# Performance work log

Measured on AMD Instinct MI355X. Metric: run time of the kernel, lower is better.

## Reference

```python
import jax, jax.numpy as jnp
import numpy as np
from jax import lax

E = 3  # num_experts

def _maxpool2(x):
    return lax.reduce_window(x, -jnp.inf, lax.max, (1, 1, 2, 2), (1, 1, 2, 2), 'VALID')

def _mixed_conv(x, experts, routing, stride, pad):
    # per-sample expert-mixed convolution via grouped conv trick
    B, Ci, H, W = x.shape
    _, Co, _, k, _ = experts.shape
    kern = jnp.einsum('be,eoikl->boikl', routing, experts).reshape(B * Co, Ci, k, k)
    y = lax.conv_general_dilated(
        x.reshape(1, B * Ci, H, W), kern, (stride, stride),
        [(pad, pad), (pad, pad)],
        dimension_numbers=('NCHW', 'OIHW', 'NCHW'),
        feature_group_count=B)
    return y.reshape(B, Co, y.shape[2], y.shape[3])

def _dyres_conv(x, experts, rw, rb, stride=1, pad=1):
    # DyRes mode 'A': routing from avg-pool + spatial-std descriptors, softmax over experts
    avg = x.mean((2, 3))
    std = x.std((2, 3))
    r = jax.nn.softmax((avg + std) @ rw.T + rb, axis=-1)  # [B, E]
    return _mixed_conv(x, experts, r, stride, pad)

def _cond_conv(x, experts, rw, rb, stride=1, pad=1):
    # CondConv: sigmoid routing from global average pool
    r = jax.nn.sigmoid(x.mean((2, 3)) @ rw.T + rb)  # [B, E]
    return _mixed_conv(x, experts, r, stride, pad)

def _conv_init(key, co, ci, k):
    return jax.random.normal(key, (E, co, ci, k, k), jnp.float32) * np.sqrt(2.0 / (ci * k * k)).astype(np.float32)

def setup_inputs() -> dict:
    key = jax.random.key(0)
    ks = jax.random.split(key, 20)
    B = 512
    d = {}
    d['x'] = jax.random.normal(ks[0], (B, 3, 32, 32), jnp.float32)
    d['dw1'] = _conv_init(ks[1], 64, 3, 3)
    d['rw1'] = jax.random.normal(ks[2], (E, 3), jnp.float32) * 0.1
    d['rb1'] = jnp.zeros((E,), jnp.float32)
    d['dw2'] = _conv_init(ks[3], 192, 64, 3)
    d['rw2'] = jax.random.normal(ks[4], (E, 64), jnp.float32) * 0.1
    d['rb2'] = jnp.zeros((E,), jnp.float32)
    d['dw3'] = _conv_init(ks[5], 384, 192, 3)
    d['rw3'] = jax.random.normal(ks[6], (E, 192), jnp.float32) * 0.1
    d['rb3'] = jnp.zeros((E,), jnp.float32)
    d['cw4'] = _conv_init(ks[7], 256, 384, 3)
    d['cr4w'] = jax.random.normal(ks[8], (E, 384), jnp.float32) * 0.1
    d['cr4b'] = jnp.zeros((E,), jnp.float32)
    d['cw5'] = _conv_init(ks[9], 256, 256, 3)
    d['cr5w'] = jax.random.normal(ks[10], (E, 256), jnp.float32) * 0.1
    d['cr5b'] = jnp.zeros((E,), jnp.float32)
    d['fw1'] = jax.random.normal(ks[11], (4096, 1024), jnp.float32) * np.sqrt(2.0 / 1024).astype(np.float32)
    d['fb1'] = jnp.zeros((4096,), jnp.float32)
    d['fw2'] = jax.random.normal(ks[12], (4096, 4096), jnp.float32) * np.sqrt(2.0 / 4096).astype(np.float32)
    d['fb2'] = jnp.zeros((4096,), jnp.float32)
    d['fw3'] = jax.random.normal(ks[13], (100, 4096), jnp.float32) * np.sqrt(1.0 / 4096).astype(np.float32)
    d['fb3'] = jnp.zeros((100,), jnp.float32)
    return d

def reference(x, dw1, rw1, rb1, dw2, rw2, rb2, dw3, rw3, rb3,
              cw4, cr4w, cr4b, cw5, cr5w, cr5b,
              fw1, fb1, fw2, fb2, fw3, fb3):
    h = jax.nn.relu(_dyres_conv(x, dw1, rw1, rb1, stride=2))   # [B,64,16,16]
    h = _maxpool2(h)                                           # [B,64,8,8]
    h = jax.nn.relu(_dyres_conv(h, dw2, rw2, rb2))             # [B,192,8,8]
    h = _maxpool2(h)                                           # [B,192,4,4]
    h = jax.nn.relu(_dyres_conv(h, dw3, rw3, rb3))             # [B,384,4,4]
    h = jax.nn.relu(_cond_conv(h, cw4, cr4w, cr4b))            # [B,256,4,4]
    h = jax.nn.relu(_cond_conv(h, cw5, cr5w, cr5b))            # [B,256,4,4]
    h = _maxpool2(h)                                           # [B,256,2,2]
    h = h.reshape(h.shape[0], -1)                              # [B,1024]
    h = jax.nn.relu(h @ fw1.T + fb1)
    h = jax.nn.relu(h @ fw2.T + fb2)
    return h @ fw3.T + fb3                                     # [B,100]
```

## Files before the change

### kernel.cpp

```cpp
#include <hip/hip_runtime.h>
#include <math.h>


typedef unsigned short u16;
typedef unsigned int u32;
typedef short bf16x8 __attribute__((ext_vector_type(8)));
typedef float f32x4 __attribute__((ext_vector_type(4)));

__device__ __forceinline__ u16 bf16_rne(float f) {
    u32 u = __float_as_uint(f);
    return (u16)((u + 0x7fffu + ((u >> 16) & 1u)) >> 16);
}
__device__ __forceinline__ u32 packsplit(float v) {
    u16 h = bf16_rne(v);
    float hf = __uint_as_float((u32)h << 16);
    u16 l = bf16_rne(v - hf);
    return ((u32)h << 16) | l;
}
__device__ __forceinline__ float unpackf(u32 p) {
    return __uint_as_float(p & 0xffff0000u) + __uint_as_float(p << 16);
}

__global__ __launch_bounds__(256)
void wsplit_kernel(const float* __restrict__ W, u16* __restrict__ whi,
                   u16* __restrict__ wlo, int total, int Kper, int Kpad)
{
    int idx = blockIdx.x * 256 + threadIdx.x;
    if (idx >= total) return;
    int r = idx / Kpad, k = idx - r * Kpad;
    float v = (k < Kper) ? W[(size_t)r * Kper + k] : 0.f;
    u16 h = bf16_rne(v);
    whi[idx] = h;
    wlo[idx] = bf16_rne(v - __uint_as_float((u32)h << 16));
}

__global__ __launch_bounds__(64)
void stats_kernel(const void* __restrict__ actv, float* __restrict__ s,
                  int Bsz, int C, int HW, int cbhw, int use_std, int packed)
{
    int idx = blockIdx.x;
    int b = idx / C, c = idx - b * C;
    size_t base = (cbhw ? ((size_t)c * Bsz + b) : ((size_t)b * C + c)) * HW;
    int lane = threadIdx.x;
    float sum = 0.f, sq = 0.f;
    if (packed) {
        const u32* p = (const u32*)actv + base;
        for (int i = lane; i < HW; i += 64) { float v = unpackf(p[i]); sum += v; sq += v * v; }
    } else {
        const float* p = (const float*)actv + base;
        for (int i = lane; i < HW; i += 64) { float v = p[i]; sum += v; sq += v * v; }
    }
#pragma unroll
    for (int off = 32; off > 0; off >>= 1) {
        sum += __shfl_down(sum, off);
        sq  += __shfl_down(sq, off);
    }
    if (lane == 0) {
        float inv = 1.f / (float)HW;
        float mean = sum * inv;
        float var = sq * inv - mean * mean;
        float outv = mean;
        if (use_std) outv += sqrtf(fmaxf(var, 0.f));
        s[idx] = outv;
    }
}

__global__ __launch_bounds__(64)
void routing_kernel(const float* __restrict__ s, const float* __restrict__ rw,
                    const float* __restrict__ rb, float* __restrict__ r,
                    int C, int softmax_mode)
{
    int b = blockIdx.x;
    int lane = threadIdx.x;
    float d0 = 0.f, d1 = 0.f, d2 = 0.f;
    for (int c = lane; c < C; c += 64) {
        float sv = s[b * C + c];
        d0 += sv * rw[c];
        d1 += sv * rw[C + c];
        d2 += sv * rw[2 * C + c];
    }
#pragma unroll
    for (int off = 32; off > 0; off >>= 1) {
        d0 += __shfl_down(d0, off);
        d1 += __shfl_down(d1, off);
        d2 += __shfl_down(d2, off);
    }
    if (lane == 0) {
        d0 += rb[0]; d1 += rb[1]; d2 += rb[2];
        if (softmax_mode) {
            float mx = fmaxf(d0, fmaxf(d1, d2));
            float e0 = expf(d0 - mx), e1 = expf(d1 - mx), e2 = expf(d2 - mx);
            float inv = 1.f / (e0 + e1 + e2);
            r[b * 3 + 0] = e0 * inv;
            r[b * 3 + 1] = e1 * inv;
            r[b * 3 + 2] = e2 * inv;
        } else {
            r[b * 3 + 0] = 1.f / (1.f + expf(-d0));
            r[b * 3 + 1] = 1.f / (1.f + expf(-d1));
            r[b * 3 + 2] = 1.f / (1.f + expf(-d2));
        }
    }
}

template<int BMODE>
__global__ __launch_bounds__(256, 2)
void cgemm_kernel(const u16* __restrict__ Whi, const u16* __restrict__ Wlo,
                  const u32* __restrict__ Bpk, const float* __restrict__ rptr,
                  float* __restrict__ Cout,
                  int M, int N, int Kper, int Kpad, int Kchunk,
                  int Ci, int Bsz, int H, int W, int lgS, int lgOW, int stride)
{
    __shared__ __align__(16) u16 Ah[2][128 * 40], Al[2][128 * 40];
    __shared__ __align__(16) u16 Bh[2][128 * 40], Bl[2][128 * 40];
    const int tid = threadIdx.x;
    const int n0 = blockIdx.x << 7, m0 = blockIdx.y << 7;
    const int kq0 = blockIdx.z * Kchunk;

    const int rowA = tid >> 1, kh16 = (tid & 1) << 4;
    const int nB = tid & 127, kOff = (tid >> 7) << 4;

    const int nn = n0 + nB;
    const int bB = nn >> lgS;
    const int sidx = nn & ((1 << lgS) - 1);
    const int ohs = (sidx >> lgOW) * stride - 1;
    const int ows = (sidx & ((1 << lgOW) - 1)) * stride - 1;
    const int chanStride = (BMODE == 2) ? H * W : Bsz * H * W;
    const long bOff = (BMODE == 2) ? (long)bB * Ci * H * W : (long)bB * H * W;
    const long nBase = bOff + (long)ohs * W + ows;

    const int lane = tid & 63, wv = tid >> 6;
    const int lm = lane & 15, qd = lane >> 4;
    const int wm = (wv & 1) << 6, wn = (wv >> 1) << 6;

    float rsv[3][4];
#pragma unroll
    for (int ni = 0; ni < 4; ++ni) {
        int n = n0 + wn + ni * 16 + lm;
        int b = n >> lgS;
#pragma unroll
        for (int e = 0; e < 3; ++e) rsv[e][ni] = rptr[b * 3 + e];
    }

    f32x4 acc[4][4], accS[4][4];
#pragma unroll
    for (int i = 0; i < 4; ++i)
#pragma unroll
        for (int j = 0; j < 4; ++j) {
            acc[i][j]  = (f32x4){0.f, 0.f, 0.f, 0.f};
            accS[i][j] = (f32x4){0.f, 0.f, 0.f, 0.f};
        }

    const int mg = m0 + rowA;
    const int nkz = Kchunk >> 5;
    const int NS = 3 * nkz;

    int eL = 0, kL = kq0;
    uint4 pA0, pA1, pA2, pA3;
    u32 pB[16];

    auto LOAD = [&]() {
        size_t aOff = ((size_t)(eL * M + mg)) * Kpad + kL + kh16;
        const u16* hp = Whi + aOff;
        const u16* lp = Wlo + aOff;
        pA0 = *(const uint4*)hp; pA1 = *(const uint4*)(hp + 8);
        pA2 = *(const uint4*)lp; pA3 = *(const uint4*)(lp + 8);
        int kb = kL + kOff;
#pragma unroll
        for (int j = 0; j < 16; ++j) {
            int k = kb + j;
            int ci = (int)((unsigned)k / 9u);
            int r9 = k - ci * 9;
            int kh = (int)(((unsigned)r9 * 11u) >> 5);
            int kw = r9 - kh * 3;
            int ih = ohs + kh, iw = ows + kw;
            u32 p = 0;
            if (k < Kper && (unsigned)ih < (unsigned)H && (unsigned)iw < (unsigned)W)
                p = Bpk[nBase + (long)ci * chanStride + kh * W + kw];
            pB[j] = p;
        }
    };
    auto ADV = [&]() {
        kL += 32;
        if (kL == kq0 + Kchunk) { kL = kq0; ++eL; }
    };
    auto STORE = [&](int buf) {
        *(uint4*)(&Ah[buf][rowA * 40 + kh16])     = pA0;
        *(uint4*)(&Ah[buf][rowA * 40 + kh16 + 8]) = pA1;
        *(uint4*)(&Al[buf][rowA * 40 + kh16])     = pA2;
        *(uint4*)(&Al[buf][rowA * 40 + kh16 + 8]) = pA3;
        u32 hw[8], lw[8];
#pragma unroll
        for (int j = 0; j < 8; ++j) {
            u32 p0 = pB[2 * j], p1 = pB[2 * j + 1];
            hw[j] = (p0 >> 16) | (p1 & 0xffff0000u);
            lw[j] = (p0 & 0xffffu) | (p1 << 16);
        }
        *(uint4*)(&Bh[buf][nB * 40 + kOff])     = make_uint4(hw[0], hw[1], hw[2], hw[3]);
        *(uint4*)(&Bh[buf][nB * 40 + kOff + 8]) = make_uint4(hw[4], hw[5], hw[6], hw[7]);
        *(uint4*)(&Bl[buf][nB * 40 + kOff])     = make_uint4(lw[0], lw[1], lw[2], lw[3]);
        *(uint4*)(&Bl[buf][nB * 40 + kOff + 8]) = make_uint4(lw[4], lw[5], lw[6], lw[7]);
    };
    auto COMPUTE = [&](int buf) {
        bf16x8 ah[4], al[4];
#pragma unroll
        for (int mi = 0; mi < 4; ++mi) {
            int row = wm + mi * 16 + lm;
            ah[mi] = *(const bf16x8*)(&Ah[buf][row * 40 + qd * 8]);
            al[mi] = *(const bf16x8*)(&Al[buf][row * 40 + qd * 8]);
        }
        __builtin_amdgcn_s_setprio(1);
#pragma unroll
        for (int ni = 0; ni < 4; ++ni) {
            int row = wn + ni * 16 + lm;
            bf16x8 bh = *(const bf16x8*)(&Bh[buf][row * 40 + qd * 8]);
            bf16x8 bl = *(const bf16x8*)(&Bl[buf][row * 40 + qd * 8]);
#pragma unroll
            for (int mi = 0; mi < 4; ++mi) {
                f32x4 c = acc[mi][ni];
                c = __builtin_amdgcn_mfma_f32_16x16x32_bf16(al[mi], bh, c, 0, 0, 0);
                c = __builtin_amdgcn_mfma_f32_16x16x32_bf16(ah[mi], bl, c, 0, 0, 0);
                c = __builtin_amdgcn_mfma_f32_16x16x32_bf16(ah[mi], bh, c, 0, 0, 0);
                acc[mi][ni] = c;
            }
        }
        __builtin_amdgcn_s_setprio(0);
    };

    LOAD(); ADV();
    int s = 0, buf = 0;
#pragma unroll
    for (int e = 0; e < 3; ++e) {
        for (int t = 0; t < nkz; ++t) {
            STORE(buf);
            if (s + 1 < NS) { LOAD(); ADV(); }
            asm volatile("s_waitcnt lgkmcnt(0)\n\ts_barrier" ::: "memory");
            COMPUTE(buf);
            buf ^= 1; ++s;
        }
#pragma unroll
        for (int mi = 0; mi < 4; ++mi)
#pragma unroll
            for (int ni = 0; ni < 4; ++ni) {
                accS[mi][ni] += acc[mi][ni] * rsv[e][ni];
                acc[mi][ni] = (f32x4){0.f, 0.f, 0.f, 0.f};
            }
    }

    const bool atom = (gridDim.z > 1);
#pragma unroll
    for (int ni = 0; ni < 4; ++ni) {
        int n = n0 + wn + ni * 16 + lm;
#pragma unroll
        for (int mi = 0; mi < 4; ++mi)
#pragma unroll
            for (int r = 0; r < 4; ++r) {
                int m = m0 + wm + mi * 16 + qd * 4 + r;
                if (m >= M) continue;
                float v = accS[mi][ni][r];
                if (atom) atomicAdd(&Cout[(size_t)m * N + n], v);
                else      Cout[(size_t)m * N + n] = v;
            }
    }
}

template<int BMODE, int BIAS, int TROUT>
__global__ __launch_bounds__(256)
void mgemm_kernel(const u16* __restrict__ Whi, const u16* __restrict__ Wlo,
                  const u32* __restrict__ Bpk, const int2* __restrict__ ktab,
                  const float* __restrict__ rptr, const float* __restrict__ bias,
                  float* __restrict__ Cout,
                  int M, int N, int Kpad, int Kchunk, int zpe,
                  int Ci, int Bsz, int H, int W, int lgS, int lgOW, int stride)
{
    __shared__ __align__(16) u16 Ah[128 * 40], Al[128 * 40];
    __shared__ __align__(16) u32 Bp[128 * 36];
    const int tid = threadIdx.x;
    const int n0 = blockIdx.x << 7, m0 = blockIdx.y << 7;
    const int bz = blockIdx.z;
    const int eA = bz / zpe;
    const int kq0 = (bz - eA * zpe) * Kchunk;

    const int rowA = tid >> 1, kh16 = (tid & 1) << 4;
    const int nB = tid & 127, kOff = (tid >> 7) << 4;

    const int lane = tid & 63, wv = tid >> 6;
    const int lm = lane & 15, qd = lane >> 4;
    const int wm = (wv & 1) << 6, wn = (wv >> 1) << 6;

    f32x4 acc[4][4];
#pragma unroll
    for (int i = 0; i < 4; ++i)
#pragma unroll
        for (int j = 0; j < 4; ++j)
            acc[i][j] = (f32x4){0.f, 0.f, 0.f, 0.f};

    const size_t aRowBase = (size_t)eA * M;

    for (int kq = kq0; kq < kq0 + Kchunk; kq += 32) {
        {
            int mg = m0 + rowA;
            uint4 h0 = {0,0,0,0}, h1 = {0,0,0,0}, l0 = {0,0,0,0}, l1 = {0,0,0,0};
            if (mg < M) {
                const u16* hp = Whi + (aRowBase + mg) * Kpad + kq + kh16;
                const u16* lp = Wlo + (aRowBase + mg) * Kpad + kq + kh16;
                h0 = *(const uint4*)hp; h1 = *(const uint4*)(hp + 8);
                l0 = *(const uint4*)lp; l1 = *(const uint4*)(lp + 8);
            }
            *(uint4*)(&Ah[rowA * 40 + kh16])     = h0;
            *(uint4*)(&Ah[rowA * 40 + kh16 + 8]) = h1;
            *(uint4*)(&Al[rowA * 40 + kh16])     = l0;
            *(uint4*)(&Al[rowA * 40 + kh16 + 8]) = l1;
        }
        {
            const u32* bp = Bpk + (size_t)(n0 + nB) * Kpad + kq + kOff;
            uint4 q0 = *(const uint4*)bp;
            uint4 q1 = *(const uint4*)(bp + 4);
            uint4 q2 = *(const uint4*)(bp + 8);
            uint4 q3 = *(const uint4*)(bp + 12);
            *(uint4*)(&Bp[nB * 36 + kOff])      = q0;
            *(uint4*)(&Bp[nB * 36 + kOff + 4])  = q1;
            *(uint4*)(&Bp[nB * 36 + kOff + 8])  = q2;
            *(uint4*)(&Bp[nB * 36 + kOff + 12]) = q3;
        }
        __syncthreads();
        {
            bf16x8 ah[4], al[4];
#pragma unroll
            for (int mi = 0; mi < 4; ++mi) {
                int row = wm + mi * 16 + lm;
                ah[mi] = *(const bf16x8*)(&Ah[row * 40 + qd * 8]);
                al[mi] = *(const bf16x8*)(&Al[row * 40 + qd * 8]);
            }
#pragma unroll
            for (int ni = 0; ni < 4; ++ni) {
                int row = wn + ni * 16 + lm;
                const u32* bp = &Bp[row * 36 + qd * 8];
                uint4 p0 = *(const uint4*)bp;
                uint4 p1 = *(const uint4*)(bp + 4);
                union { u32 w[4]; bf16x8 v; } bh, bl;
                bh.w[0] = (p0.x >> 16) | (p0.y & 0xffff0000u);
                bl.w[0] = (p0.x & 0xffffu) | (p0.y << 16);
                bh.w[1] = (p0.z >> 16) | (p0.w & 0xffff0000u);
                bl.w[1] = (p0.z & 0xffffu) | (p0.w << 16);
                bh.w[2] = (p1.x >> 16) | (p1.y & 0xffff0000u);
                bl.w[2] = (p1.x & 0xffffu) | (p1.y << 16);
                bh.w[3] = (p1.z >> 16) | (p1.w & 0xffff0000u);
                bl.w[3] = (p1.z & 0xffffu) | (p1.w << 16);
#pragma unroll
                for (int mi = 0; mi < 4; ++mi) {
                    f32x4 c = acc[mi][ni];
                    c = __builtin_amdgcn_mfma_f32_16x16x32_bf16(al[mi], bh.v, c, 0, 0, 0);
                    c = __builtin_amdgcn_mfma_f32_16x16x32_bf16(ah[mi], bl.v, c, 0, 0, 0);
                    c = __builtin_amdgcn_mfma_f32_16x16x32_bf16(ah[mi], bh.v, c, 0, 0, 0);
                    acc[mi][ni] = c;
                }
            }
        }
        __syncthreads();
    }

#pragma unroll
    for (int ni = 0; ni < 4; ++ni) {
        int n = n0 + wn + ni * 16 + lm;
        if (n >= N) continue;
#pragma unroll
        for (int mi = 0; mi < 4; ++mi)
#pragma unroll
            for (int r = 0; r < 4; ++r) {
                int m = m0 + wm + mi * 16 + qd * 4 + r;
                if (m >= M) continue;
                float v = acc[mi][ni][r];
                if (BIAS && bz == 0) v += bias[m];
                if (TROUT) atomicAdd(&Cout[(size_t)n * M + m], v);
                else       atomicAdd(&Cout[(size_t)m * N + n], v);
            }
    }
}

__global__ __launch_bounds__(256)
void pack_kernel(const float* __restrict__ in, u32* __restrict__ outp,
                 int count, int relu)
{
    int i = blockIdx.x * 256 + threadIdx.x;
    if (i >= count) return;
    float v = in[i];
    if (relu) v = fmaxf(v, 0.f);
    outp[i] = packsplit(v);
}

template<int RELU>
__global__ __launch_bounds__(256)
void pool_pack_kernel(const float* __restrict__ in, u32* __restrict__ outp,
                      int CB, int H, int W)
{
    int OH = H >> 1, OW = W >> 1;
    int total = CB * OH * OW;
    int i = blockIdx.x * 256 + threadIdx.x;
    if (i >= total) return;
    int ow = i % OW;
    int t = i / OW;
    int oh = t % OH;
    int cb = t / OH;
    const float* p = in + ((size_t)cb * H + (oh << 1)) * W + (ow << 1);
    float v = fmaxf(fmaxf(p[0], p[1]), fmaxf(p[W], p[W + 1]));
    if (RELU) v = fmaxf(v, 0.f);
    outp[i] = packsplit(v);
}

__global__ __launch_bounds__(256)
void pool_flatten_pack_kernel(const float* __restrict__ in, u32* __restrict__ outp)
{
    int i = blockIdx.x * 256 + threadIdx.x;
    if (i >= 512 * 1024) return;
    int b = i >> 10;
    int f = i & 1023;
    int c = f >> 2, s = f & 3;
    int oh = s >> 1, ow = s & 1;
    const float* p = in + (((size_t)c * 512 + b) * 4 + (oh << 1)) * 4 + (ow << 1);
    float v = fmaxf(fmaxf(p[0], p[1]), fmaxf(p[4], p[5]));
    outp[i] = packsplit(fmaxf(v, 0.f));
}

__global__ __launch_bounds__(256)
void tp_pack_kernel(const float* __restrict__ in, u32* __restrict__ outp,
                    int Mt, int Nt)
{
    __shared__ float t[32][33];
    int tx = threadIdx.x & 31, ty = threadIdx.x >> 5;
    int mB = blockIdx.x << 5, nB = blockIdx.y << 5;
#pragma unroll
    for (int i = 0; i < 4; ++i) {
        int mm = ty + i * 8;
        t[mm][tx] = in[(size_t)(mB + mm) * Nt + nB + tx];
    }
    __syncthreads();
#pragma unroll
    for (int i = 0; i < 4; ++i) {
        int nn = ty + i * 8;
        float v = fmaxf(t[tx][nn], 0.f);
        outp[(size_t)(nB + nn) * Mt + mB + tx] = packsplit(v);
    }
}

extern "C" void kernel_launch(void* const* d_in, const int* in_sizes, int n_in,
                              void* d_out, int out_size, void* d_ws, size_t ws_size,
                              hipStream_t stream)
{
    const float* x    = (const float*)d_in[0];
    const float* dw1  = (const float*)d_in[1];
    const float* rw1  = (const float*)d_in[2];
    const float* rb1  = (const float*)d_in[3];
    const float* dw2  = (const float*)d_in[4];
    const float* rw2  = (const float*)d_in[5];
    const float* rb2  = (const float*)d_in[6];
    const float* dw3  = (const float*)d_in[7];
    const float* rw3  = (const float*)d_in[8];
    const float* rb3  = (const float*)d_in[9];
    const float* cw4  = (const float*)d_in[10];
    const float* cr4w = (const float*)d_in[11];
    const float* cr4b = (const float*)d_in[12];
    const float* cw5  = (const float*)d_in[13];
    const float* cr5w = (const float*)d_in[14];
    const float* cr5b = (const float*)d_in[15];
    const float* fw1  = (const float*)d_in[16];
    const float* fb1  = (const float*)d_in[17];
    const float* fw2  = (const float*)d_in[18];
    const float* fb2  = (const float*)d_in[19];
    const float* fw3  = (const float*)d_in[20];
    const float* fb3  = (const float*)d_in[21];
    float* out = (float*)d_out;

    float* ws    = (float*)d_ws;
    float* r1    = ws;
    float* r2    = r1 + 1536;
    float* r3    = r2 + 1536;
    float* r4    = r3 + 1536;
    float* r5    = r4 + 1536;
    float* sdesc = ws + 8192 + 65536;
    const size_t REGION = 18874368;
    float* region = sdesc + 196608;
    float* slab   = region;
    u16*   regEnd = (u16*)(region + REGION);
    u32*   P1     = (u32*)(region + REGION);
    u32*   P2     = P1 + 3145728;

    u16 *w1h = regEnd - 2*(size_t)6144,     *w1l = regEnd - (size_t)6144;
    u16 *w2h = regEnd - 2*(size_t)331776,   *w2l = regEnd - (size_t)331776;
    u16 *w3h = regEnd - 2*(size_t)1990656,  *w3l = regEnd - (size_t)1990656;
    u16 *w4h = regEnd - 2*(size_t)2654208,  *w4l = regEnd - (size_t)2654208;
    u16 *w5h = regEnd - 2*(size_t)1769472,  *w5l = regEnd - (size_t)1769472;
    u16 *f1h = regEnd - 2*(size_t)4194304,  *f1l = regEnd - (size_t)4194304;
    u16 *f2h = regEnd - 2*(size_t)16777216, *f2l = regEnd - (size_t)16777216;
    u16 *f3h = regEnd - 2*(size_t)409600,   *f3l = regEnd - (size_t)409600;

    u32* xpk   = P1;
    u32* a1pk  = P2;
    u32* a2pk  = P1;
    u32* c3pk  = P2;
    u32* c4pk  = P1;
    u32* hTpk  = P2;
    u32* f1pkT = P1;
    u32* f2pkT = P2;

    const int B = 512;

    pack_kernel<<<6144, 256, 0, stream>>>(x, xpk, 1572864, 0);

    wsplit_kernel<<<24, 256, 0, stream>>>(dw1, w1h, w1l, 6144, 27, 32);
    stats_kernel<<<B * 3, 64, 0, stream>>>(x, sdesc, B, 3, 1024, 0, 1, 0);
    routing_kernel<<<B, 64, 0, stream>>>(sdesc, rw1, rb1, r1, 3, 1);
    cgemm_kernel<2><<<dim3(1024, 1, 1), 256, 0, stream>>>(
        w1h, w1l, xpk, r1, slab, 64, 131072, 27, 32, 32, 3, B, 32, 32, 8, 4, 2);
    pool_pack_kernel<1><<<8192, 256, 0, stream>>>(slab, a1pk, 64 * 512, 16, 16);

    wsplit_kernel<<<1296, 256, 0, stream>>>(dw2, w2h, w2l, 331776, 576, 576);
    stats_kernel<<<B * 64, 64, 0, stream>>>(a1pk, sdesc, B, 64, 64, 1, 1, 1);
    routing_kernel<<<B, 64, 0, stream>>>(sdesc, rw2, rb2, r2, 64, 1);
    cgemm_kernel<1><<<dim3(256, 2, 1), 256, 0, stream>>>(
        w2h, w2l, a1pk, r2, slab, 192, 32768, 576, 576, 576, 64, B, 8, 8, 6, 3, 1);
    pool_pack_kernel<1><<<6144, 256, 0, stream>>>(slab, a2pk, 192 * 512, 8, 8);

    wsplit_kernel<<<7776, 256, 0, stream>>>(dw3, w3h, w3l, 1990656, 1728, 1728);
    stats_kernel<<<B * 192, 64, 0, stream>>>(a2pk, sdesc, B, 192, 16, 1, 1, 1);
    routing_kernel<<<B, 64, 0, stream>>>(sdesc, rw3, rb3, r3, 192, 1);
    hipMemsetAsync(slab, 0, (size_t)384 * 8192 * 4, stream);
    cgemm_kernel<1><<<dim3(64, 3, 2), 256, 0, stream>>>(
        w3h, w3l, a2pk, r3, slab, 384, 8192, 1728, 1728, 864, 192, B, 4, 4, 4, 2, 1);
    pack_kernel<<<12288, 256, 0, stream>>>(slab, c3pk, 3145728, 1);

    wsplit_kernel<<<10368, 256, 0, stream>>>(cw4, w4h, w4l, 2654208, 3456, 3456);
    stats_kernel<<<B * 384, 64, 0, stream>>>(c3pk, sdesc, B, 384, 16, 1, 0, 1);
    routing_kernel<<<B, 64, 0, stream>>>(sdesc, cr4w, cr4b, r4, 384, 0);
    hipMemsetAsync(slab, 0, (size_t)256 * 8192 * 4, stream);
    cgemm_kernel<1><<<dim3(64, 2, 4), 256, 0, stream>>>(
        w4h, w4l, c3pk, r4, slab, 256, 8192, 3456, 3456, 864, 384, B, 4, 4, 4, 2, 1);
    pack_kernel<<<8192, 256, 0, stream>>>(slab, c4pk, 2097152, 1);

    wsplit_kernel<<<6912, 256, 0, stream>>>(cw5, w5h, w5l, 1769472, 2304, 2304);
    stats_kernel<<<B * 256, 64, 0, stream>>>(c4pk, sdesc, B, 256, 16, 1, 0, 1);
    routing_kernel<<<B, 64, 0, stream>>>(sdesc, cr5w, cr5b, r5, 256, 0);
    hipMemsetAsync(slab, 0, (size_t)256 * 8192 * 4, stream);
    cgemm_kernel<1><<<dim3(64, 2, 4), 256, 0, stream>>>(
        w5h, w5l, c4pk, r5, slab, 256, 8192, 2304, 2304, 576, 256, B, 4, 4, 4, 2, 1);

    pool_flatten_pack_kernel<<<2048, 256, 0, stream>>>(slab, hTpk);

    wsplit_kernel<<<16384, 256, 0, stream>>>(fw1, f1h, f1l, 4194304, 1024, 1024);
    hipMemsetAsync(slab, 0, (size_t)4096 * 512 * 4, stream);
    mgemm_kernel<0, 1, 0><<<dim3(4, 32, 8), 256, 0, stream>>>(
        f1h, f1l, hTpk, nullptr, nullptr, fb1, slab, 4096, 512, 1024, 128, 8, 0, 0, 0, 0, 0, 0, 0);
    tp_pack_kernel<<<dim3(128, 16), 256, 0, stream>>>(slab, f1pkT, 4096, 512);

    wsplit_kernel<<<65536, 256, 0, stream>>>(fw2, f2h, f2l, 16777216, 4096, 4096);
    hipMemsetAsync(slab, 0, (size_t)4096 * 512 * 4, stream);
    mgemm_kernel<0, 1, 0><<<dim3(4, 32, 8), 256, 0, stream>>>(
        f2h, f2l, f1pkT, nullptr, nullptr, fb2, slab, 4096, 512, 4096, 512, 8, 0, 0, 0, 0, 0, 0, 0);
    tp_pack_kernel<<<dim3(128, 16), 256, 0, stream>>>(slab, f2pkT, 4096, 512);

    wsplit_kernel<<<1600, 256, 0, stream>>>(fw3, f3h, f3l, 409600, 4096, 4096);
    hipMemsetAsync(out, 0, (size_t)512 * 100 * 4, stream);
    mgemm_kernel<0, 1, 1><<<dim3(4, 1, 32), 256, 0, stream>>>(
        f3h, f3l, f2pkT, nullptr, nullptr, fb3, out, 100, 512, 4096, 128, 32, 0, 0, 0, 0, 0, 0, 0);
}
```

Before: 1.496 ms.

## Switch conv activations to padded channels-last layout with vectorized im2col loads

Conv layers 2-5 now store activations in a zero-padded NHWC packed layout. Weights are reordered so K runs over (cell, channel), which lets each thread fetch 16 contiguous B values with four 16-byte loads instead of 16 bounds-checked scalar gathers with div/mod. The GEMM output is written channels-last, and the pool, pack and stats kernels are rewritten to match. Block indices are also swizzled across XCDs. The trade-off is extra padding memory and a stats kernel that runs one thread per channel with serial loops.

```diff
diff --git a/kernel.cpp b/kernel.cpp
--- a/kernel.cpp
+++ b/kernel.cpp
@@ -19,6 +19,11 @@
 }
 __device__ __forceinline__ float unpackf(u32 p) {
     return __uint_as_float(p & 0xffff0000u) + __uint_as_float(p << 16);
+}
+__device__ __forceinline__ int xcd_swz(int bid, int n) {
+    if ((n & 7) != 0) return bid;
+    int cpx = n >> 3;
+    return (bid & 7) * cpx + (bid >> 3);
 }
 
 __global__ __launch_bounds__(256)
@@ -34,22 +39,31 @@
     wlo[idx] = bf16_rne(v - __uint_as_float((u32)h << 16));
 }
 
+__global__ __launch_bounds__(256)
+void wsplit_cl_kernel(const float* __restrict__ W, u16* __restrict__ whi,
+                      u16* __restrict__ wlo, int total, int Ci)
+{
+    int idx = blockIdx.x * 256 + threadIdx.x;
+    if (idx >= total) return;
+    int Kper = 9 * Ci;
+    int r = idx / Kper, kp = idx - r * Kper;
+    int cell = kp / Ci, ci = kp - cell * Ci;
+    float v = W[(size_t)r * Kper + ci * 9 + cell];
+    u16 h = bf16_rne(v);
+    whi[idx] = h;
+    wlo[idx] = bf16_rne(v - __uint_as_float((u32)h << 16));
+}
+
 __global__ __launch_bounds__(64)
-void stats_kernel(const void* __restrict__ actv, float* __restrict__ s,
-                  int Bsz, int C, int HW, int cbhw, int use_std, int packed)
+void stats_kernel(const float* __restrict__ actv, float* __restrict__ s,
+                  int C, int HW, int use_std)
 {
     int idx = blockIdx.x;
-    int b = idx / C, c = idx - b * C;
-    size_t base = (cbhw ? ((size_t)c * Bsz + b) : ((size_t)b * C + c)) * HW;
+    size_t base = (size_t)idx * HW;
     int lane = threadIdx.x;
     float sum = 0.f, sq = 0.f;
-    if (packed) {
-        const u32* p = (const u32*)actv + base;
-        for (int i = lane; i < HW; i += 64) { float v = unpackf(p[i]); sum += v; sq += v * v; }
-    } else {
-        const float* p = (const float*)actv + base;
-        for (int i = lane; i < HW; i += 64) { float v = p[i]; sum += v; sq += v * v; }
-    }
+    const float* p = actv + base;
+    for (int i = lane; i < HW; i += 64) { float v = p[i]; sum += v; sq += v * v; }
 #pragma unroll
     for (int off = 32; off > 0; off >>= 1) {
         sum += __shfl_down(sum, off);
@@ -63,6 +77,26 @@
         if (use_std) outv += sqrtf(fmaxf(var, 0.f));
         s[idx] = outv;
     }
+}
+
+__global__ __launch_bounds__(384)
+void stats_cl_kernel(const u32* __restrict__ act, float* __restrict__ s,
+                     int H2, int W2, int C, int use_std)
+{
+    int b = blockIdx.x, c = threadIdx.x;
+    int Hin = H2 - 2, Win = W2 - 2;
+    float sum = 0.f, sq = 0.f;
+    for (int h = 0; h < Hin; ++h)
+        for (int w = 0; w < Win; ++w) {
+            float v = unpackf(act[(((size_t)b * H2 + h + 1) * W2 + w + 1) * C + c]);
+            sum += v; sq += v * v;
+        }
+    float inv = 1.f / (float)(Hin * Win);
+    float mean = sum * inv;
+    float var = sq * inv - mean * mean;
+    float outv = mean;
+    if (use_std) outv += sqrtf(fmaxf(var, 0.f));
+    s[b * C + c] = outv;
 }
 
 __global__ __launch_bounds__(64)
@@ -102,31 +136,27 @@
     }
 }
 
-template<int BMODE>
+template<int CI, int H2, int W2, int LGS, int LGOW>
 __global__ __launch_bounds__(256, 2)
-void cgemm_kernel(const u16* __restrict__ Whi, const u16* __restrict__ Wlo,
-                  const u32* __restrict__ Bpk, const float* __restrict__ rptr,
-                  float* __restrict__ Cout,
-                  int M, int N, int Kper, int Kpad, int Kchunk,
-                  int Ci, int Bsz, int H, int W, int lgS, int lgOW, int stride)
+void cgemm_cl_kernel(const u16* __restrict__ Whi, const u16* __restrict__ Wlo,
+                     const u32* __restrict__ Bpk, const float* __restrict__ rptr,
+                     float* __restrict__ Cout, int M, int N, int Kper, int Kchunk)
 {
     __shared__ __align__(16) u16 Ah[2][128 * 40], Al[2][128 * 40];
     __shared__ __align__(16) u16 Bh[2][128 * 40], Bl[2][128 * 40];
     const int tid = threadIdx.x;
-    const int n0 = blockIdx.x << 7, m0 = blockIdx.y << 7;
+    const int bx = xcd_swz(blockIdx.x, gridDim.x);
+    const int n0 = bx << 7, m0 = blockIdx.y << 7;
     const int kq0 = blockIdx.z * Kchunk;
 
     const int rowA = tid >> 1, kh16 = (tid & 1) << 4;
     const int nB = tid & 127, kOff = (tid >> 7) << 4;
 
     const int nn = n0 + nB;
-    const int bB = nn >> lgS;
-    const int sidx = nn & ((1 << lgS) - 1);
-    const int ohs = (sidx >> lgOW) * stride - 1;
-    const int ows = (sidx & ((1 << lgOW) - 1)) * stride - 1;
-    const int chanStride = (BMODE == 2) ? H * W : Bsz * H * W;
-    const long bOff = (BMODE == 2) ? (long)bB * Ci * H * W : (long)bB * H * W;
-    const long nBase = bOff + (long)ohs * W + ows;
+    const int bB = nn >> LGS;
+    const int sidx = nn & ((1 << LGS) - 1);
+    const int oh = sidx >> LGOW, ow = sidx & ((1 << LGOW) - 1);
+    const long nBase = ((long)(bB * H2 + oh) * W2 + ow) * CI;
 
     const int lane = tid & 63, wv = tid >> 6;
     const int lm = lane & 15, qd = lane >> 4;
@@ -136,7 +166,7 @@
 #pragma unroll
     for (int ni = 0; ni < 4; ++ni) {
         int n = n0 + wn + ni * 16 + lm;
-        int b = n >> lgS;
+        int b = n >> LGS;
 #pragma unroll
         for (int e = 0; e < 3; ++e) rsv[e][ni] = rptr[b * 3 + e];
     }
@@ -156,28 +186,24 @@
 
     int eL = 0, kL = kq0;
     uint4 pA0, pA1, pA2, pA3;
-    u32 pB[16];
+    uint4 pQ0, pQ1, pQ2, pQ3;
 
     auto LOAD = [&]() {
-        size_t aOff = ((size_t)(eL * M + mg)) * Kpad + kL + kh16;
+        size_t aOff = ((size_t)(eL * M + mg)) * Kper + kL + kh16;
         const u16* hp = Whi + aOff;
         const u16* lp = Wlo + aOff;
         pA0 = *(const uint4*)hp; pA1 = *(const uint4*)(hp + 8);
         pA2 = *(const uint4*)lp; pA3 = *(const uint4*)(lp + 8);
-        int kb = kL + kOff;
-#pragma unroll
-        for (int j = 0; j < 16; ++j) {
-            int k = kb + j;
-            int ci = (int)((unsigned)k / 9u);
-            int r9 = k - ci * 9;
-            int kh = (int)(((unsigned)r9 * 11u) >> 5);
-            int kw = r9 - kh * 3;
-            int ih = ohs + kh, iw = ows + kw;
-            u32 p = 0;
-            if (k < Kper && (unsigned)ih < (unsigned)H && (unsigned)iw < (unsigned)W)
-                p = Bpk[nBase + (long)ci * chanStride + kh * W + kw];
-            pB[j] = p;
-        }
+        int k = kL + kOff;
+        int cell = k / CI;
+        int ci0 = k - cell * CI;
+        int kh = (cell * 11) >> 5;
+        int kw = cell - kh * 3;
+        const u32* bp = Bpk + (nBase + (long)((kh * W2 + kw) * CI + ci0));
+        pQ0 = *(const uint4*)bp;
+        pQ1 = *(const uint4*)(bp + 4);
+        pQ2 = *(const uint4*)(bp + 8);
+        pQ3 = *(const uint4*)(bp + 12);
     };
     auto ADV = [&]() {
         kL += 32;
@@ -188,10 +214,12 @@
         *(uint4*)(&Ah[buf][rowA * 40 + kh16 + 8]) = pA1;
         *(uint4*)(&Al[buf][rowA * 40 + kh16])     = pA2;
         *(uint4*)(&Al[buf][rowA * 40 + kh16 + 8]) = pA3;
+        u32 qv[16] = {pQ0.x, pQ0.y, pQ0.z, pQ0.w, pQ1.x, pQ1.y, pQ1.z, pQ1.w,
+                      pQ2.x, pQ2.y, pQ2.z, pQ2.w, pQ3.x, pQ3.y, pQ3.z, pQ3.w};
         u32 hw[8], lw[8];
 #pragma unroll
         for (int j = 0; j < 8; ++j) {
-            u32 p0 = pB[2 * j], p1 = pB[2 * j + 1];
+            u32 p0 = qv[2 * j], p1 = qv[2 * j + 1];
             hw[j] = (p0 >> 16) | (p1 & 0xffff0000u);
             lw[j] = (p0 & 0xffffu) | (p1 << 16);
         }
@@ -257,28 +285,170 @@
                 int m = m0 + wm + mi * 16 + qd * 4 + r;
                 if (m >= M) continue;
                 float v = accS[mi][ni][r];
-                if (atom) atomicAdd(&Cout[(size_t)m * N + n], v);
-                else      Cout[(size_t)m * N + n] = v;
-            }
-    }
-}
-
-template<int BMODE, int BIAS, int TROUT>
+                if (atom) atomicAdd(&Cout[(size_t)n * M + m], v);
+                else      Cout[(size_t)n * M + m] = v;
+            }
+    }
+}
+
+__global__ __launch_bounds__(256, 2)
+void cgemm_l1_kernel(const u16* __restrict__ Whi, const u16* __restrict__ Wlo,
+                     const u32* __restrict__ Bpk, const float* __restrict__ rptr,
+                     float* __restrict__ Cout, int M, int N)
+{
+    __shared__ __align__(16) u16 Ah[2][128 * 40], Al[2][128 * 40];
+    __shared__ __align__(16) u16 Bh[2][128 * 40], Bl[2][128 * 40];
+    const int tid = threadIdx.x;
+    const int bx = xcd_swz(blockIdx.x, gridDim.x);
+    const int n0 = bx << 7;
+    const int Kper = 27, Kpad = 32;
+    const int H = 32, W = 32;
+
+    const int rowA = tid >> 1, kh16 = (tid & 1) << 4;
+    const int nB = tid & 127, kOff = (tid >> 7) << 4;
+
+    const int nn = n0 + nB;
+    const int bB = nn >> 8;
+    const int sidx = nn & 255;
+    const int ohs = (sidx >> 4) * 2 - 1;
+    const int ows = (sidx & 15) * 2 - 1;
+    const long nBase = (long)bB * 3072 + (long)ohs * W + ows;
+
+    const int lane = tid & 63, wv = tid >> 6;
+    const int lm = lane & 15, qd = lane >> 4;
+    const int wm = (wv & 1) << 6, wn = (wv >> 1) << 6;
+
+    float rsv[3][4];
+#pragma unroll
+    for (int ni = 0; ni < 4; ++ni) {
+        int n = n0 + wn + ni * 16 + lm;
+        int b = n >> 8;
+#pragma unroll
+        for (int e = 0; e < 3; ++e) rsv[e][ni] = rptr[b * 3 + e];
+    }
+
+    f32x4 acc[4][4], accS[4][4];
+#pragma unroll
+    for (int i = 0; i < 4; ++i)
+#pragma unroll
+        for (int j = 0; j < 4; ++j) {
+            acc[i][j]  = (f32x4){0.f, 0.f, 0.f, 0.f};
+            accS[i][j] = (f32x4){0.f, 0.f, 0.f, 0.f};
+        }
+
+    const int mg = rowA;
+    int eL = 0;
+    uint4 pA0, pA1, pA2, pA3;
+    u32 pB[16];
+
+    auto LOAD = [&]() {
+        size_t aOff = ((size_t)(eL * M + mg)) * Kpad + kh16;
+        const u16* hp = Whi + aOff;
+        const u16* lp = Wlo + aOff;
+        pA0 = *(const uint4*)hp; pA1 = *(const uint4*)(hp + 8);
+        pA2 = *(const uint4*)lp; pA3 = *(const uint4*)(lp + 8);
+#pragma unroll
+        for (int j = 0; j < 16; ++j) {
+            int k = kOff + j;
+            int ci = (int)((unsigned)k / 9u);
+            int r9 = k - ci * 9;
+            int kh = (int)(((unsigned)r9 * 11u) >> 5);
+            int kw = r9 - kh * 3;
+            int ih = ohs + kh, iw = ows + kw;
+            u32 p = 0;
+            if (k < Kper && (unsigned)ih < (unsigned)H && (unsigned)iw < (unsigned)W)
+                p = Bpk[nBase + (long)ci * 1024 + kh * W + kw];
+            pB[j] = p;
+        }
+    };
+    auto STORE = [&](int buf) {
+        *(uint4*)(&Ah[buf][rowA * 40 + kh16])     = pA0;
+        *(uint4*)(&Ah[buf][rowA * 40 + kh16 + 8]) = pA1;
+        *(uint4*)(&Al[buf][rowA * 40 + kh16])     = pA2;
+        *(uint4*)(&Al[buf][rowA * 40 + kh16 + 8]) = pA3;
+        u32 hw[8], lw[8];
+#pragma unroll
+        for (int j = 0; j < 8; ++j) {
+            u32 p0 = pB[2 * j], p1 = pB[2 * j + 1];
+            hw[j] = (p0 >> 16) | (p1 & 0xffff0000u);
+            lw[j] = (p0 & 0xffffu) | (p1 << 16);
+        }
+        *(uint4*)(&Bh[buf][nB * 40 + kOff])     = make_uint4(hw[0], hw[1], hw[2], hw[3]);
+        *(uint4*)(&Bh[buf][nB * 40 + kOff + 8]) = make_uint4(hw[4], hw[5], hw[6], hw[7]);
+        *(uint4*)(&Bl[buf][nB * 40 + kOff])     = make_uint4(lw[0], lw[1], lw[2], lw[3]);
+        *(uint4*)(&Bl[buf][nB * 40 + kOff + 8]) = make_uint4(lw[4], lw[5], lw[6], lw[7]);
+    };
+    auto COMPUTE = [&](int buf) {
+        bf16x8 ah[4], al[4];
+#pragma unroll
+        for (int mi = 0; mi < 4; ++mi) {
+            int row = wm + mi * 16 + lm;
+            ah[mi] = *(const bf16x8*)(&Ah[buf][row * 40 + qd * 8]);
+            al[mi] = *(const bf16x8*)(&Al[buf][row * 40 + qd * 8]);
+        }
+        __builtin_amdgcn_s_setprio(1);
+#pragma unroll
+        for (int ni = 0; ni < 4; ++ni) {
+            int row = wn + ni * 16 + lm;
+            bf16x8 bh = *(const bf16x8*)(&Bh[buf][row * 40 + qd * 8]);
+            bf16x8 bl = *(const bf16x8*)(&Bl[buf][row * 40 + qd * 8]);
+#pragma unroll
+            for (int mi = 0; mi < 4; ++mi) {
+                f32x4 c = acc[mi][ni];
+                c = __builtin_amdgcn_mfma_f32_16x16x32_bf16(al[mi], bh, c, 0, 0, 0);
+                c = __builtin_amdgcn_mfma_f32_16x16x32_bf16(ah[mi], bl, c, 0, 0, 0);
+                c = __builtin_amdgcn_mfma_f32_16x16x32_bf16(ah[mi], bh, c, 0, 0, 0);
+                acc[mi][ni] = c;
+            }
+        }
+        __builtin_amdgcn_s_setprio(0);
+    };
+
+    LOAD(); ++eL;
+    int buf = 0;
+#pragma unroll
+    for (int e = 0; e < 3; ++e) {
+        STORE(buf);
+        if (e < 2) { LOAD(); ++eL; }
+        asm volatile("s_waitcnt lgkmcnt(0)\n\ts_barrier" ::: "memory");
+        COMPUTE(buf);
+        buf ^= 1;
+#pragma unroll
+        for (int mi = 0; mi < 4; ++mi)
+#pragma unroll
+            for (int ni = 0; ni < 4; ++ni) {
+                accS[mi][ni] += acc[mi][ni] * rsv[e][ni];
+                acc[mi][ni] = (f32x4){0.f, 0.f, 0.f, 0.f};
+            }
+    }
+
+#pragma unroll
+    for (int ni = 0; ni < 4; ++ni) {
+        int n = n0 + wn + ni * 16 + lm;
+#pragma unroll
+        for (int mi = 0; mi < 4; ++mi)
+#pragma unroll
+            for (int r = 0; r < 4; ++r) {
+                int m = wm + mi * 16 + qd * 4 + r;
+                if (m >= M) continue;
+                Cout[(size_t)n * M + m] = accS[mi][ni][r];
+            }
+    }
+}
+
+template<int BIAS, int TROUT>
 __global__ __launch_bounds__(256)
 void mgemm_kernel(const u16* __restrict__ Whi, const u16* __restrict__ Wlo,
-                  const u32* __restrict__ Bpk, const int2* __restrict__ ktab,
-                  const float* __restrict__ rptr, const float* __restrict__ bias,
+                  const u32* __restrict__ Bpk, const float* __restrict__ bias,
                   float* __restrict__ Cout,
-                  int M, int N, int Kpad, int Kchunk, int zpe,
-                  int Ci, int Bsz, int H, int W, int lgS, int lgOW, int stride)
+                  int M, int N, int Kpad, int Kchunk)
 {
     __shared__ __align__(16) u16 Ah[128 * 40], Al[128 * 40];
     __shared__ __align__(16) u32 Bp[128 * 36];
     const int tid = threadIdx.x;
     const int n0 = blockIdx.x << 7, m0 = blockIdx.y << 7;
     const int bz = blockIdx.z;
-    const int eA = bz / zpe;
-    const int kq0 = (bz - eA * zpe) * Kchunk;
+    const int kq0 = bz * Kchunk;
 
     const int rowA = tid >> 1, kh16 = (tid & 1) << 4;
     const int nB = tid & 127, kOff = (tid >> 7) << 4;
@@ -293,16 +463,14 @@
 #pragma unroll
         for (int j = 0; j < 4; ++j)
             acc[i][j] = (f32x4){0.f, 0.f, 0.f, 0.f};
-
-    const size_t aRowBase = (size_t)eA * M;
 
     for (int kq = kq0; kq < kq0 + Kchunk; kq += 32) {
         {
             int mg = m0 + rowA;
             uint4 h0 = {0,0,0,0}, h1 = {0,0,0,0}, l0 = {0,0,0,0}, l1 = {0,0,0,0};
             if (mg < M) {
-                const u16* hp = Whi + (aRowBase + mg) * Kpad + kq + kh16;
-                const u16* lp = Wlo + (aRowBase + mg) * Kpad + kq + kh16;
+                const u16* hp = Whi + (size_t)mg * Kpad + kq + kh16;
+                const u16* lp = Wlo + (size_t)mg * Kpad + kq + kh16;
                 h0 = *(const uint4*)hp; h1 = *(const uint4*)(hp + 8);
                 l0 = *(const uint4*)lp; l1 = *(const uint4*)(lp + 8);
             }
@@ -378,46 +546,65 @@
 }
 
 __global__ __launch_bounds__(256)
-void pack_kernel(const float* __restrict__ in, u32* __restrict__ outp,
-                 int count, int relu)
+void pack_kernel(const float* __restrict__ in, u32* __restrict__ outp, int count)
 {
     int i = blockIdx.x * 256 + threadIdx.x;
     if (i >= count) return;
-    float v = in[i];
-    if (relu) v = fmaxf(v, 0.f);
-    outp[i] = packsplit(v);
-}
-
-template<int RELU>
+    outp[i] = packsplit(in[i]);
+}
+
 __global__ __launch_bounds__(256)
-void pool_pack_kernel(const float* __restrict__ in, u32* __restrict__ outp,
-                      int CB, int H, int W)
-{
-    int OH = H >> 1, OW = W >> 1;
-    int total = CB * OH * OW;
+void pool_pack_cl_kernel(const float* __restrict__ in, u32* __restrict__ outp,
+                         int Bn, int Hin, int Win, int C)
+{
+    int OH = Hin >> 1, OW = Win >> 1, H2 = OH + 2, W2 = OW + 2;
+    int total = Bn * H2 * W2 * C;
     int i = blockIdx.x * 256 + threadIdx.x;
     if (i >= total) return;
-    int ow = i % OW;
-    int t = i / OW;
-    int oh = t % OH;
-    int cb = t / OH;
-    const float* p = in + ((size_t)cb * H + (oh << 1)) * W + (ow << 1);
-    float v = fmaxf(fmaxf(p[0], p[1]), fmaxf(p[W], p[W + 1]));
-    if (RELU) v = fmaxf(v, 0.f);
-    outp[i] = packsplit(v);
+    int c = i % C; int t = i / C;
+    int w = t % W2; t /= W2;
+    int h = t % H2; int b = t / H2;
+    u32 pv = 0;
+    if (h >= 1 && h <= OH && w >= 1 && w <= OW) {
+        int oh = h - 1, ow = w - 1;
+        const float* p = in + (((size_t)b * Hin + 2 * oh) * Win + 2 * ow) * C + c;
+        size_t rs = (size_t)Win * C;
+        float v = fmaxf(fmaxf(p[0], p[C]), fmaxf(p[rs], p[rs + C]));
+        pv = packsplit(fmaxf(v, 0.f));
+    }
+    outp[i] = pv;
 }
 
 __global__ __launch_bounds__(256)
-void pool_flatten_pack_kernel(const float* __restrict__ in, u32* __restrict__ outp)
+void pack_cl_kernel(const float* __restrict__ in, u32* __restrict__ outp,
+                    int Bn, int Hin, int Win, int C)
+{
+    int H2 = Hin + 2, W2 = Win + 2;
+    int total = Bn * H2 * W2 * C;
+    int i = blockIdx.x * 256 + threadIdx.x;
+    if (i >= total) return;
+    int c = i % C; int t = i / C;
+    int w = t % W2; t /= W2;
+    int h = t % H2; int b = t / H2;
+    u32 pv = 0;
+    if (h >= 1 && h <= Hin && w >= 1 && w <= Win) {
+        float v = in[(((size_t)b * Hin + (h - 1)) * Win + (w - 1)) * C + c];
+        pv = packsplit(fmaxf(v, 0.f));
+    }
+    outp[i] = pv;
+}
+
+__global__ __launch_bounds__(256)
+void pool_flatten_cl_kernel(const float* __restrict__ in, u32* __restrict__ outp)
 {
     int i = blockIdx.x * 256 + threadIdx.x;
     if (i >= 512 * 1024) return;
     int b = i >> 10;
     int f = i & 1023;
-    int c = f >> 2, s = f & 3;
-    int oh = s >> 1, ow = s & 1;
-    const float* p = in + (((size_t)c * 512 + b) * 4 + (oh << 1)) * 4 + (ow << 1);
-    float v = fmaxf(fmaxf(p[0], p[1]), fmaxf(p[4], p[5]));
+    int c = f >> 2, sp = f & 3;
+    int oh = sp >> 1, ow = sp & 1;
+    const float* p = in + (((size_t)b * 4 + 2 * oh) * 4 + 2 * ow) * 256 + c;
+    float v = fmaxf(fmaxf(p[0], p[256]), fmaxf(p[1024], p[1024 + 256]));
     outp[i] = packsplit(fmaxf(v, 0.f));
 }
 
@@ -480,9 +667,9 @@
     const size_t REGION = 18874368;
     float* region = sdesc + 196608;
     float* slab   = region;
+    u32*   a3u    = (u32*)(region + 4194304);
     u16*   regEnd = (u16*)(region + REGION);
     u32*   P1     = (u32*)(region + REGION);
-    u32*   P2     = P1 + 3145728;
 
     u16 *w1h = regEnd - 2*(size_t)6144,     *w1l = regEnd - (size_t)6144;
     u16 *w2h = regEnd - 2*(size_t)331776,   *w2l = regEnd - (size_t)331776;
@@ -494,71 +681,70 @@
     u16 *f3h = regEnd - 2*(size_t)409600,   *f3l = regEnd - (size_t)409600;
 
     u32* xpk   = P1;
-    u32* a1pk  = P2;
-    u32* a2pk  = P1;
-    u32* c3pk  = P2;
-    u32* c4pk  = P1;
-    u32* hTpk  = P2;
-    u32* f1pkT = P1;
-    u32* f2pkT = P2;
+    u32* a1    = P1;
+    u32* a2    = P1;
+    u32* a4    = P1;
+    u32* hTpk  = P1;
+    u32* f1pkT = P1 + 1048576;
+    u32* f2pkT = P1 + 3145728;
 
     const int B = 512;
 
-    pack_kernel<<<6144, 256, 0, stream>>>(x, xpk, 1572864, 0);
+    pack_kernel<<<6144, 256, 0, stream>>>(x, xpk, 1572864);
 
     wsplit_kernel<<<24, 256, 0, stream>>>(dw1, w1h, w1l, 6144, 27, 32);
-    stats_kernel<<<B * 3, 64, 0, stream>>>(x, sdesc, B, 3, 1024, 0, 1, 0);
+    stats_kernel<<<B * 3, 64, 0, stream>>>(x, sdesc, 3, 1024, 1);
     routing_kernel<<<B, 64, 0, stream>>>(sdesc, rw1, rb1, r1, 3, 1);
-    cgemm_kernel<2><<<dim3(1024, 1, 1), 256, 0, stream>>>(
-        w1h, w1l, xpk, r1, slab, 64, 131072, 27, 32, 32, 3, B, 32, 32, 8, 4, 2);
-    pool_pack_kernel<1><<<8192, 256, 0, stream>>>(slab, a1pk, 64 * 512, 16, 16);
-
-    wsplit_kernel<<<1296, 256, 0, stream>>>(dw2, w2h, w2l, 331776, 576, 576);
-    stats_kernel<<<B * 64, 64, 0, stream>>>(a1pk, sdesc, B, 64, 64, 1, 1, 1);
+    cgemm_l1_kernel<<<dim3(1024, 1, 1), 256, 0, stream>>>(
+        w1h, w1l, xpk, r1, slab, 64, 131072);
+    pool_pack_cl_kernel<<<12800, 256, 0, stream>>>(slab, a1, B, 16, 16, 64);
+
+    wsplit_cl_kernel<<<1296, 256, 0, stream>>>(dw2, w2h, w2l, 331776, 64);
+    stats_cl_kernel<<<B, 64, 0, stream>>>(a1, sdesc, 10, 10, 64, 1);
     routing_kernel<<<B, 64, 0, stream>>>(sdesc, rw2, rb2, r2, 64, 1);
-    cgemm_kernel<1><<<dim3(256, 2, 1), 256, 0, stream>>>(
-        w2h, w2l, a1pk, r2, slab, 192, 32768, 576, 576, 576, 64, B, 8, 8, 6, 3, 1);
-    pool_pack_kernel<1><<<6144, 256, 0, stream>>>(slab, a2pk, 192 * 512, 8, 8);
-
-    wsplit_kernel<<<7776, 256, 0, stream>>>(dw3, w3h, w3l, 1990656, 1728, 1728);
-    stats_kernel<<<B * 192, 64, 0, stream>>>(a2pk, sdesc, B, 192, 16, 1, 1, 1);
+    cgemm_cl_kernel<64, 10, 10, 6, 3><<<dim3(256, 2, 1), 256, 0, stream>>>(
+        w2h, w2l, a1, r2, slab, 192, 32768, 576, 576);
+    pool_pack_cl_kernel<<<13824, 256, 0, stream>>>(slab, a2, B, 8, 8, 192);
+
+    wsplit_cl_kernel<<<7776, 256, 0, stream>>>(dw3, w3h, w3l, 1990656, 192);
+    stats_cl_kernel<<<B, 192, 0, stream>>>(a2, sdesc, 6, 6, 192, 1);
     routing_kernel<<<B, 64, 0, stream>>>(sdesc, rw3, rb3, r3, 192, 1);
-    hipMemsetAsync(slab, 0, (size_t)384 * 8192 * 4, stream);
-    cgemm_kernel<1><<<dim3(64, 3, 2), 256, 0, stream>>>(
-        w3h, w3l, a2pk, r3, slab, 384, 8192, 1728, 1728, 864, 192, B, 4, 4, 4, 2, 1);
-    pack_kernel<<<12288, 256, 0, stream>>>(slab, c3pk, 3145728, 1);
-
-    wsplit_kernel<<<10368, 256, 0, stream>>>(cw4, w4h, w4l, 2654208, 3456, 3456);
-    stats_kernel<<<B * 384, 64, 0, stream>>>(c3pk, sdesc, B, 384, 16, 1, 0, 1);
+    hipMemsetAsync(slab, 0, (size_t)8192 * 384 * 4, stream);
+    cgemm_cl_kernel<192, 6, 6, 4, 2><<<dim3(64, 3, 2), 256, 0, stream>>>(
+        w3h, w3l, a2, r3, slab, 384, 8192, 1728, 864);
+    pack_cl_kernel<<<27648, 256, 0, stream>>>(slab, a3u, B, 4, 4, 384);
+
+    wsplit_cl_kernel<<<10368, 256, 0, stream>>>(cw4, w4h, w4l, 2654208, 384);
+    stats_cl_kernel<<<B, 384, 0, stream>>>(a3u, sdesc, 6, 6, 384, 0);
     routing_kernel<<<B, 64, 0, stream>>>(sdesc, cr4w, cr4b, r4, 384, 0);
-    hipMemsetAsync(slab, 0, (size_t)256 * 8192 * 4, stream);
-    cgemm_kernel<1><<<dim3(64, 2, 4), 256, 0, stream>>>(
-        w4h, w4l, c3pk, r4, slab, 256, 8192, 3456, 3456, 864, 384, B, 4, 4, 4, 2, 1);
-    pack_kernel<<<8192, 256, 0, stream>>>(slab, c4pk, 2097152, 1);
-
-    wsplit_kernel<<<6912, 256, 0, stream>>>(cw5, w5h, w5l, 1769472, 2304, 2304);
-    stats_kernel<<<B * 256, 64, 0, stream>>>(c4pk, sdesc, B, 256, 16, 1, 0, 1);
+    hipMemsetAsync(slab, 0, (size_t)8192 * 256 * 4, stream);
+    cgemm_cl_kernel<384, 6, 6, 4, 2><<<dim3(64, 2, 4), 256, 0, stream>>>(
+        w4h, w4l, a3u, r4, slab, 256, 8192, 3456, 864);
+    pack_cl_kernel<<<18432, 256, 0, stream>>>(slab, a4, B, 4, 4, 256);
+
+    wsplit_cl_kernel<<<6912, 256, 0, stream>>>(cw5, w5h, w5l, 1769472, 256);
+    stats_cl_kernel<<<B, 256, 0, stream>>>(a4, sdesc, 6, 6, 256, 0);
     routing_kernel<<<B, 64, 0, stream>>>(sdesc, cr5w, cr5b, r5, 256, 0);
-    hipMemsetAsync(slab, 0, (size_t)256 * 8192 * 4, stream);
-    cgemm_kernel<1><<<dim3(64, 2, 4), 256, 0, stream>>>(
-        w5h, w5l, c4pk, r5, slab, 256, 8192, 2304, 2304, 576, 256, B, 4, 4, 4, 2, 1);
-
-    pool_flatten_pack_kernel<<<2048, 256, 0, stream>>>(slab, hTpk);
+    hipMemsetAsync(slab, 0, (size_t)8192 * 256 * 4, stream);
+    cgemm_cl_kernel<256, 6, 6, 4, 2><<<dim3(64, 2, 4), 256, 0, stream>>>(
+        w5h, w5l, a4, r5, slab, 256, 8192, 2304, 576);
+
+    pool_flatten_cl_kernel<<<2048, 256, 0, stream>>>(slab, hTpk);
 
     wsplit_kernel<<<16384, 256, 0, stream>>>(fw1, f1h, f1l, 4194304, 1024, 1024);
     hipMemsetAsync(slab, 0, (size_t)4096 * 512 * 4, stream);
-    mgemm_kernel<0, 1, 0><<<dim3(4, 32, 8), 256, 0, stream>>>(
-        f1h, f1l, hTpk, nullptr, nullptr, fb1, slab, 4096, 512, 1024, 128, 8, 0, 0, 0, 0, 0, 0, 0);
+    mgemm_kernel<1, 0><<<dim3(4, 32, 8), 256, 0, stream>>>(
+        f1h, f1l, hTpk, fb1, slab, 4096, 512, 1024, 128);
     tp_pack_kernel<<<dim3(128, 16), 256, 0, stream>>>(slab, f1pkT, 4096, 512);
 
     wsplit_kernel<<<65536, 256, 0, stream>>>(fw2, f2h, f2l, 16777216, 4096, 4096);
     hipMemsetAsync(slab, 0, (size_t)4096 * 512 * 4, stream);
-    mgemm_kernel<0, 1, 0><<<dim3(4, 32, 8), 256, 0, stream>>>(
-        f2h, f2l, f1pkT, nullptr, nullptr, fb2, slab, 4096, 512, 4096, 512, 8, 0, 0, 0, 0, 0, 0, 0);
+    mgemm_kernel<1, 0><<<dim3(4, 32, 8), 256, 0, stream>>>(
+        f2h, f2l, f1pkT, fb2, slab, 4096, 512, 4096, 512);
     tp_pack_kernel<<<dim3(128, 16), 256, 0, stream>>>(slab, f2pkT, 4096, 512);
 
     wsplit_kernel<<<1600, 256, 0, stream>>>(fw3, f3h, f3l, 409600, 4096, 4096);
     hipMemsetAsync(out, 0, (size_t)512 * 100 * 4, stream);
-    mgemm_kernel<0, 1, 1><<<dim3(4, 1, 32), 256, 0, stream>>>(
-        f3h, f3l, f2pkT, nullptr, nullptr, fb3, out, 100, 512, 4096, 128, 32, 0, 0, 0, 0, 0, 0, 0);
-}
+    mgemm_kernel<1, 1><<<dim3(4, 1, 32), 256, 0, stream>>>(
+        f3h, f3l, f2pkT, fb3, out, 100, 512, 4096, 128);
+}
```

Measured after the change: 1.473 ms. Within noise of the previous version (-1.5%).
